# Optimization experiments

Measured on AMD Instinct MI355X. Metric: run time of the kernel, lower is better.

Reference implementation:

```python
import jax, jax.numpy as jnp
import numpy as np

N_NODES = 40000
N_EDGES = 640000
IN_CH = 128
HID_CH = 256
EDGE_DIM = 64
N_SAMP = 2048
T = 1.0
EPS_GIN = 0.0
EPS_NORM = 1e-12


def setup_inputs() -> dict:
    key = jax.random.key(0)
    ks = jax.random.split(key, 12)
    x = jax.random.normal(ks[0], (N_NODES, IN_CH), dtype=jnp.float32)
    edge_index = jax.random.randint(ks[1], (2, N_EDGES), 0, N_NODES, dtype=jnp.int64)
    edge_attr = jax.random.normal(ks[2], (N_EDGES, EDGE_DIM), dtype=jnp.float32)
    pos_ind = jax.random.randint(ks[3], (N_SAMP,), 0, N_NODES, dtype=jnp.int64)
    neg_ind = jax.random.randint(ks[4], (N_SAMP,), 0, N_NODES, dtype=jnp.int64)
    # GINEConv internal edge projection Linear(64 -> 128)
    We = jax.random.normal(ks[5], (EDGE_DIM, IN_CH), dtype=jnp.float32) / np.sqrt(EDGE_DIM)
    be = jnp.zeros((IN_CH,), dtype=jnp.float32)
    # MLP: Linear(128->256), ReLU, Linear(256->256)
    W1 = jax.random.normal(ks[6], (IN_CH, HID_CH), dtype=jnp.float32) / np.sqrt(IN_CH)
    b1 = jnp.zeros((HID_CH,), dtype=jnp.float32)
    W2 = jax.random.normal(ks[7], (HID_CH, HID_CH), dtype=jnp.float32) / np.sqrt(HID_CH)
    b2 = jnp.zeros((HID_CH,), dtype=jnp.float32)
    thresholding_node = jax.random.normal(ks[8], (1, HID_CH), dtype=jnp.float32)
    return {"x": x, "edge_index": edge_index, "edge_attr": edge_attr,
            "pos_ind": pos_ind, "neg_ind": neg_ind,
            "We": We, "be": be, "W1": W1, "b1": b1, "W2": W2, "b2": b2,
            "thresholding_node": thresholding_node}


def _normalize(v):
    n = jnp.linalg.norm(v, axis=-1, keepdims=True)
    return v / jnp.maximum(n, EPS_NORM)


def reference(x, edge_index, edge_attr, pos_ind, neg_ind,
              We, be, W1, b1, W2, b2, thresholding_node):
    src, dst = edge_index[0], edge_index[1]  # PyG: message from x_j (src) to target i (dst)
    edge_emb = edge_attr @ We + be                    # [E, in_ch]
    msg = jax.nn.relu(x[src] + edge_emb)              # gather + add + relu
    agg = jax.ops.segment_sum(msg, dst, num_segments=x.shape[0])  # scatter-add
    h = (1.0 + EPS_GIN) * x + agg
    emb = jax.nn.relu(h @ W1 + b1) @ W2 + b2          # [N, hid]

    center = _normalize(emb[0])                       # [hid]
    pos = _normalize(emb[pos_ind])                    # [P, hid]
    neg = _normalize(emb[neg_ind])                    # [Q, hid]
    thr = _normalize(thresholding_node)               # [1, hid]

    pos_score_mean = (center[None, :] * pos).sum(-1).mean(-1)
    neg_score_mean = (center[None, :] * neg).sum(-1).mean(-1)
    thr_score = (center * thr).sum(-1)                # [1]

    pos_loss = jnp.log(jnp.clip(jax.nn.sigmoid((pos_score_mean - thr_score) / T), 1e-12)).mean()
    neg_loss = jnp.log(jnp.clip(jax.nn.sigmoid((thr_score - neg_score_mean) / T), 1e-12)).mean()
    return -pos_loss - neg_loss
```

## Files before the change

### kernel.cpp

```cpp
#include <hip/hip_runtime.h>
#include <math.h>

#define N_NODES 40000
#define N_EDGES 640000
#define IN_CH 128
#define HID_CH 256
#define EDGE_DIM 64
#define N_SAMP 2048
#define NSEL (1 + 2 * N_SAMP)
#define MAXU 4097
#define HBUCKETS 5120
#define CAP 64
#define MROWS 8

__global__ __launch_bounds__(256) void init_kernel(
    int* __restrict__ slot, int* __restrict__ counters, int* __restrict__ hist)
{
    const int i = blockIdx.x * 256 + threadIdx.x;
    if (i < 40960) slot[i] = -1;
    if (i < HBUCKETS) hist[i] = 0;
    if (i < 32) counters[i] = 0;
}

__global__ __launch_bounds__(256) void flag_kernel(
    const int* __restrict__ pos, const int* __restrict__ neg,
    int* __restrict__ slot, int* __restrict__ counters)
{
    int r = blockIdx.x * 256 + threadIdx.x;
    if (r >= NSEL) return;
    int node = (r == 0) ? 0 : (r <= N_SAMP ? pos[r - 1] : neg[r - 1 - N_SAMP]);
    int old = atomicCAS(&slot[node], -1, -2);
    if (old == -1) slot[node] = atomicAdd(&counters[1], 1);
}

__global__ __launch_bounds__(256) void bucket_kernel(
    const int* __restrict__ ei, const int* __restrict__ slot,
    int* __restrict__ hist, int2* __restrict__ bucket)
{
    const int e = blockIdx.x * 256 + threadIdx.x;
    const int d = ei[N_EDGES + e];
    const int sl = slot[d];
    if (sl >= 0) {
        int p = atomicAdd(&hist[sl], 1);
        if (p < CAP) bucket[(size_t)sl * CAP + p] = make_int2(e, ei[e]);
    }
}

__global__ __launch_bounds__(256) void edge_kernel(
    const float* __restrict__ x, const float* __restrict__ edge_attr,
    const float* __restrict__ We, const float* __restrict__ be,
    const int* __restrict__ hist, const int2* __restrict__ bucket,
    float* __restrict__ agg_c)
{
    __shared__ float sWe[EDGE_DIM * IN_CH];
    __shared__ float sA[4][8][EDGE_DIM];
    __shared__ int scnt[4];
    const int tid = threadIdx.x, wave = tid >> 6, lane = tid & 63;

    {
        const float4* s4 = (const float4*)We;
        float4* d4 = (float4*)sWe;
        for (int i = tid; i < (EDGE_DIM * IN_CH) / 4; i += 256) d4[i] = s4[i];
    }
    const int s = blockIdx.x * 4 + wave;
    const int cnt = min(hist[s], CAP);
    if (lane == 0) scnt[wave] = cnt;
    __syncthreads();
    const int cmax = max(max(scnt[0], scnt[1]), max(scnt[2], scnt[3]));

    const float be0 = be[lane], be1 = be[64 + lane];
    const int2* bk = bucket + (size_t)min(s, MAXU - 1) * CAP;
    float sum0 = 0.f, sum1 = 0.f;

    for (int c0 = 0; c0 < cmax; c0 += 8) {
        int2 bv = make_int2(0, 0);
        {
            int jj = lane & 7;
            if (c0 + jj < cnt) bv = bk[c0 + jj];
        }
#pragma unroll
        for (int j = 0; j < 8; ++j) {
            int e = __shfl(bv.x, j);
            float a = 0.f;
            if (c0 + j < cnt) a = edge_attr[(size_t)e * EDGE_DIM + lane];
            sA[wave][j][lane] = a;
        }
        float xr0[8], xr1[8];
#pragma unroll
        for (int j = 0; j < 8; ++j) {
            int src = __shfl(bv.y, j);
            bool v = (c0 + j < cnt);
            size_t off = (size_t)src * IN_CH;
            xr0[j] = v ? x[off + lane] : 0.f;
            xr1[j] = v ? x[off + 64 + lane] : 0.f;
        }
        __syncthreads();

        float acc0[8], acc1[8];
#pragma unroll
        for (int j = 0; j < 8; ++j) { acc0[j] = 0.f; acc1[j] = 0.f; }
        for (int k0 = 0; k0 < EDGE_DIM; k0 += 4) {
            float w0[4], w1[4];
#pragma unroll
            for (int kk = 0; kk < 4; ++kk) {
                w0[kk] = sWe[(k0 + kk) * IN_CH + lane];
                w1[kk] = sWe[(k0 + kk) * IN_CH + 64 + lane];
            }
#pragma unroll
            for (int j = 0; j < 8; ++j) {
                float4 a = *(const float4*)&sA[wave][j][k0];
                acc0[j] += a.x * w0[0] + a.y * w0[1] + a.z * w0[2] + a.w * w0[3];
                acc1[j] += a.x * w1[0] + a.y * w1[1] + a.z * w1[2] + a.w * w1[3];
            }
        }
#pragma unroll
        for (int j = 0; j < 8; ++j) {
            if (c0 + j < cnt) {
                sum0 += fmaxf(xr0[j] + acc0[j] + be0, 0.f);
                sum1 += fmaxf(xr1[j] + acc1[j] + be1, 0.f);
            }
        }
        __syncthreads();
    }
    agg_c[(size_t)s * IN_CH + lane] = sum0;
    agg_c[(size_t)s * IN_CH + 64 + lane] = sum1;
}

__global__ __launch_bounds__(256) void mlp_kernel(
    const float* __restrict__ x, const float* __restrict__ agg_c,
    const int* __restrict__ slot, const int* __restrict__ pos,
    const int* __restrict__ neg, const float* __restrict__ W1,
    const float* __restrict__ b1, const float* __restrict__ W2,
    const float* __restrict__ b2, float* __restrict__ emb)
{
    __shared__ float sin_[MROWS][IN_CH];
    __shared__ float shid[MROWS][HID_CH];
    __shared__ int snode[MROWS], sslot[MROWS];
    const int tid = threadIdx.x;
    const int r0 = blockIdx.x * MROWS;
    if (tid < MROWS) {
        int r = r0 + tid;
        int node = 0;
        if (r < NSEL && r > 0) node = (r <= N_SAMP) ? pos[r - 1] : neg[r - 1 - N_SAMP];
        snode[tid] = node;
        sslot[tid] = slot[node];
    }
    __syncthreads();
    {
        int rr = tid >> 5, k4 = tid & 31;
        int n = snode[rr], sl = sslot[rr];
        float4 xa = ((const float4*)(x + (size_t)n * IN_CH))[k4];
        float4 ga = ((const float4*)(agg_c + (size_t)sl * IN_CH))[k4];
        ((float4*)sin_[rr])[k4] =
            make_float4(xa.x + ga.x, xa.y + ga.y, xa.z + ga.z, xa.w + ga.w);
    }
    __syncthreads();

    float acc[MROWS];
#pragma unroll
    for (int rr = 0; rr < MROWS; ++rr) acc[rr] = 0.f;
    for (int k0 = 0; k0 < IN_CH; k0 += 4) {
        float w[4];
#pragma unroll
        for (int kk = 0; kk < 4; ++kk) w[kk] = W1[(k0 + kk) * HID_CH + tid];
#pragma unroll
        for (int rr = 0; rr < MROWS; ++rr) {
            float4 h = *(const float4*)&sin_[rr][k0];
            acc[rr] += h.x * w[0] + h.y * w[1] + h.z * w[2] + h.w * w[3];
        }
    }
    float bb1 = b1[tid];
#pragma unroll
    for (int rr = 0; rr < MROWS; ++rr) shid[rr][tid] = fmaxf(acc[rr] + bb1, 0.f);
    __syncthreads();

#pragma unroll
    for (int rr = 0; rr < MROWS; ++rr) acc[rr] = 0.f;
    for (int k0 = 0; k0 < HID_CH; k0 += 4) {
        float w[4];
#pragma unroll
        for (int kk = 0; kk < 4; ++kk) w[kk] = W2[(k0 + kk) * HID_CH + tid];
#pragma unroll
        for (int rr = 0; rr < MROWS; ++rr) {
            float4 h = *(const float4*)&shid[rr][k0];
            acc[rr] += h.x * w[0] + h.y * w[1] + h.z * w[2] + h.w * w[3];
        }
    }
    float bb2 = b2[tid];
#pragma unroll
    for (int rr = 0; rr < MROWS; ++rr) {
        int r = r0 + rr;
        if (r < NSEL) emb[(size_t)r * HID_CH + tid] = acc[rr] + bb2;
    }
}

__global__ __launch_bounds__(256) void score_kernel(
    const float* __restrict__ emb, float* __restrict__ partial)
{
    const int tid = threadIdx.x;
    const int wave = tid >> 6, lane = tid & 63;
    const int rid = blockIdx.x * 4 + wave;
    const float4 c = ((const float4*)emb)[lane];
    const float4 v = ((const float4*)(emb + (size_t)(rid + 1) * HID_CH))[lane];
    float cc = c.x * c.x + c.y * c.y + c.z * c.z + c.w * c.w;
    float vv = v.x * v.x + v.y * v.y + v.z * v.z + v.w * v.w;
    float cv = c.x * v.x + c.y * v.y + c.z * v.z + c.w * v.w;
#pragma unroll
    for (int off = 32; off; off >>= 1) {
        cc += __shfl_xor(cc, off, 64);
        vv += __shfl_xor(vv, off, 64);
        cv += __shfl_xor(cv, off, 64);
    }
    float score = cv / (fmaxf(sqrtf(cc), 1e-12f) * fmaxf(sqrtf(vv), 1e-12f));
    __shared__ float wsum[4];
    if (lane == 0) wsum[wave] = score;
    __syncthreads();
    if (tid == 0) partial[blockIdx.x] = wsum[0] + wsum[1] + wsum[2] + wsum[3];
}

__global__ __launch_bounds__(64) void loss_kernel(
    const float* __restrict__ emb, const float* __restrict__ thrn,
    const float* __restrict__ partial, float* __restrict__ out)
{
    const int lane = threadIdx.x;
    const float4 c = ((const float4*)emb)[lane];
    const float4 t = ((const float4*)thrn)[lane];
    float cc = c.x * c.x + c.y * c.y + c.z * c.z + c.w * c.w;
    float tt = t.x * t.x + t.y * t.y + t.z * t.z + t.w * t.w;
    float ct = c.x * t.x + c.y * t.y + c.z * t.z + c.w * t.w;
    float ps = 0.f, ns = 0.f;
#pragma unroll
    for (int i = 0; i < 8; ++i) ps += partial[lane + 64 * i];
#pragma unroll
    for (int i = 0; i < 8; ++i) ns += partial[512 + lane + 64 * i];
#pragma unroll
    for (int off = 32; off; off >>= 1) {
        cc += __shfl_xor(cc, off, 64);
        tt += __shfl_xor(tt, off, 64);
        ct += __shfl_xor(ct, off, 64);
        ps += __shfl_xor(ps, off, 64);
        ns += __shfl_xor(ns, off, 64);
    }
    if (lane == 0) {
        float thr = ct / (fmaxf(sqrtf(cc), 1e-12f) * fmaxf(sqrtf(tt), 1e-12f));
        float pm = ps / (float)N_SAMP;
        float nm = ns / (float)N_SAMP;
        float s1 = 1.f / (1.f + expf(-(pm - thr)));
        float s2 = 1.f / (1.f + expf(-(thr - nm)));
        s1 = fmaxf(s1, 1e-12f);
        s2 = fmaxf(s2, 1e-12f);
        out[0] = -(logf(s1) + logf(s2));
    }
}

extern "C" void kernel_launch(void* const* d_in, const int* in_sizes, int n_in,
                              void* d_out, int out_size, void* d_ws, size_t ws_size,
                              hipStream_t stream)
{
    const float* x         = (const float*)d_in[0];
    const int*   ei        = (const int*)d_in[1];
    const float* edge_attr = (const float*)d_in[2];
    const int*   pos       = (const int*)d_in[3];
    const int*   neg       = (const int*)d_in[4];
    const float* We        = (const float*)d_in[5];
    const float* be        = (const float*)d_in[6];
    const float* W1        = (const float*)d_in[7];
    const float* b1        = (const float*)d_in[8];
    const float* W2        = (const float*)d_in[9];
    const float* b2        = (const float*)d_in[10];
    const float* thrn      = (const float*)d_in[11];
    float* out = (float*)d_out;

    int* slot     = (int*)d_ws;
    int* counters = slot + 40960;
    int* hist     = counters + 32;
    int2* bucket  = (int2*)(hist + HBUCKETS);
    float* agg_c  = (float*)(bucket + (size_t)MAXU * CAP);
    float* emb    = agg_c + 4100 * IN_CH;
    float* partial= emb + (size_t)NSEL * HID_CH;

    init_kernel<<<160, 256, 0, stream>>>(slot, counters, hist);
    flag_kernel<<<(NSEL + 255) / 256, 256, 0, stream>>>(pos, neg, slot, counters);
    bucket_kernel<<<N_EDGES / 256, 256, 0, stream>>>(ei, slot, hist, bucket);
    edge_kernel<<<1025, 256, 0, stream>>>(x, edge_attr, We, be, hist, bucket, agg_c);
    mlp_kernel<<<(NSEL + MROWS - 1) / MROWS, 256, 0, stream>>>(x, agg_c, slot, pos, neg,
                                                               W1, b1, W2, b2, emb);
    score_kernel<<<1024, 256, 0, stream>>>(emb, partial);
    loss_kernel<<<1, 64, 0, stream>>>(emb, thrn, partial, out);
}
```

Before: 336.7 us.

## Replace block barriers in edge kernel with per-wave sync; fuse loss into score kernel

In the edge aggregation kernel, each wave now loops over its own bucket count and uses its private shared-memory tile. Block-wide __syncthreads inside the loop are replaced by s_waitcnt lgkmcnt(0) plus a scheduling barrier, so waves with few edges no longer wait on the block's maximum. The separate single-block loss kernel is folded into the score kernel, where the last block to finish (found with an atomic counter and threadfence) computes the final loss, saving one launch. The counter-based completion relies on counters being zeroed by init_kernel on every call.

```diff
diff --git a/kernel.cpp b/kernel.cpp
--- a/kernel.cpp
+++ b/kernel.cpp
@@ -54,7 +54,6 @@
 {
     __shared__ float sWe[EDGE_DIM * IN_CH];
     __shared__ float sA[4][8][EDGE_DIM];
-    __shared__ int scnt[4];
     const int tid = threadIdx.x, wave = tid >> 6, lane = tid & 63;
 
     {
@@ -62,17 +61,17 @@
         float4* d4 = (float4*)sWe;
         for (int i = tid; i < (EDGE_DIM * IN_CH) / 4; i += 256) d4[i] = s4[i];
     }
+    __syncthreads();
+
     const int s = blockIdx.x * 4 + wave;
     const int cnt = min(hist[s], CAP);
-    if (lane == 0) scnt[wave] = cnt;
-    __syncthreads();
-    const int cmax = max(max(scnt[0], scnt[1]), max(scnt[2], scnt[3]));
-
     const float be0 = be[lane], be1 = be[64 + lane];
     const int2* bk = bucket + (size_t)min(s, MAXU - 1) * CAP;
+    float (*myA)[EDGE_DIM] = sA[wave];
     float sum0 = 0.f, sum1 = 0.f;
 
-    for (int c0 = 0; c0 < cmax; c0 += 8) {
+    for (int c0 = 0; c0 < cnt; c0 += 8) {
+        asm volatile("s_waitcnt lgkmcnt(0)" ::: "memory");
         int2 bv = make_int2(0, 0);
         {
             int jj = lane & 7;
@@ -83,7 +82,7 @@
             int e = __shfl(bv.x, j);
             float a = 0.f;
             if (c0 + j < cnt) a = edge_attr[(size_t)e * EDGE_DIM + lane];
-            sA[wave][j][lane] = a;
+            myA[j][lane] = a;
         }
         float xr0[8], xr1[8];
 #pragma unroll
@@ -94,7 +93,8 @@
             xr0[j] = v ? x[off + lane] : 0.f;
             xr1[j] = v ? x[off + 64 + lane] : 0.f;
         }
-        __syncthreads();
+        asm volatile("s_waitcnt lgkmcnt(0)" ::: "memory");
+        __builtin_amdgcn_sched_barrier(0);
 
         float acc0[8], acc1[8];
 #pragma unroll
@@ -108,7 +108,7 @@
             }
 #pragma unroll
             for (int j = 0; j < 8; ++j) {
-                float4 a = *(const float4*)&sA[wave][j][k0];
+                float4 a = *(const float4*)&myA[j][k0];
                 acc0[j] += a.x * w0[0] + a.y * w0[1] + a.z * w0[2] + a.w * w0[3];
                 acc1[j] += a.x * w1[0] + a.y * w1[1] + a.z * w1[2] + a.w * w1[3];
             }
@@ -120,7 +120,6 @@
                 sum1 += fmaxf(xr1[j] + acc1[j] + be1, 0.f);
             }
         }
-        __syncthreads();
     }
     agg_c[(size_t)s * IN_CH + lane] = sum0;
     agg_c[(size_t)s * IN_CH + 64 + lane] = sum1;
@@ -195,8 +194,12 @@
 }
 
 __global__ __launch_bounds__(256) void score_kernel(
-    const float* __restrict__ emb, float* __restrict__ partial)
-{
+    const float* __restrict__ emb, const float* __restrict__ thrn,
+    float* __restrict__ partial, int* __restrict__ counters,
+    float* __restrict__ out)
+{
+    __shared__ float wsum[4];
+    __shared__ int sdone;
     const int tid = threadIdx.x;
     const int wave = tid >> 6, lane = tid & 63;
     const int rid = blockIdx.x * 4 + wave;
@@ -212,44 +215,45 @@
         cv += __shfl_xor(cv, off, 64);
     }
     float score = cv / (fmaxf(sqrtf(cc), 1e-12f) * fmaxf(sqrtf(vv), 1e-12f));
-    __shared__ float wsum[4];
     if (lane == 0) wsum[wave] = score;
     __syncthreads();
-    if (tid == 0) partial[blockIdx.x] = wsum[0] + wsum[1] + wsum[2] + wsum[3];
-}
-
-__global__ __launch_bounds__(64) void loss_kernel(
-    const float* __restrict__ emb, const float* __restrict__ thrn,
-    const float* __restrict__ partial, float* __restrict__ out)
-{
-    const int lane = threadIdx.x;
-    const float4 c = ((const float4*)emb)[lane];
-    const float4 t = ((const float4*)thrn)[lane];
-    float cc = c.x * c.x + c.y * c.y + c.z * c.z + c.w * c.w;
-    float tt = t.x * t.x + t.y * t.y + t.z * t.z + t.w * t.w;
-    float ct = c.x * t.x + c.y * t.y + c.z * t.z + c.w * t.w;
-    float ps = 0.f, ns = 0.f;
-#pragma unroll
-    for (int i = 0; i < 8; ++i) ps += partial[lane + 64 * i];
-#pragma unroll
-    for (int i = 0; i < 8; ++i) ns += partial[512 + lane + 64 * i];
-#pragma unroll
-    for (int off = 32; off; off >>= 1) {
-        cc += __shfl_xor(cc, off, 64);
-        tt += __shfl_xor(tt, off, 64);
-        ct += __shfl_xor(ct, off, 64);
-        ps += __shfl_xor(ps, off, 64);
-        ns += __shfl_xor(ns, off, 64);
-    }
-    if (lane == 0) {
-        float thr = ct / (fmaxf(sqrtf(cc), 1e-12f) * fmaxf(sqrtf(tt), 1e-12f));
-        float pm = ps / (float)N_SAMP;
-        float nm = ns / (float)N_SAMP;
-        float s1 = 1.f / (1.f + expf(-(pm - thr)));
-        float s2 = 1.f / (1.f + expf(-(thr - nm)));
-        s1 = fmaxf(s1, 1e-12f);
-        s2 = fmaxf(s2, 1e-12f);
-        out[0] = -(logf(s1) + logf(s2));
+    if (tid == 0) {
+        partial[blockIdx.x] = wsum[0] + wsum[1] + wsum[2] + wsum[3];
+        __threadfence();
+        int old = atomicAdd(&counters[2], 1);
+        sdone = (old == 1023) ? 1 : 0;
+    }
+    __syncthreads();
+    if (sdone && tid < 64) {
+        __threadfence();
+        const float4 cc4 = ((const float4*)emb)[tid];
+        const float4 t = ((const float4*)thrn)[tid];
+        float c2 = cc4.x * cc4.x + cc4.y * cc4.y + cc4.z * cc4.z + cc4.w * cc4.w;
+        float tt = t.x * t.x + t.y * t.y + t.z * t.z + t.w * t.w;
+        float ct = cc4.x * t.x + cc4.y * t.y + cc4.z * t.z + cc4.w * t.w;
+        float ps = 0.f, ns = 0.f;
+#pragma unroll
+        for (int i = 0; i < 8; ++i) ps += partial[tid + 64 * i];
+#pragma unroll
+        for (int i = 0; i < 8; ++i) ns += partial[512 + tid + 64 * i];
+#pragma unroll
+        for (int off = 32; off; off >>= 1) {
+            c2 += __shfl_xor(c2, off, 64);
+            tt += __shfl_xor(tt, off, 64);
+            ct += __shfl_xor(ct, off, 64);
+            ps += __shfl_xor(ps, off, 64);
+            ns += __shfl_xor(ns, off, 64);
+        }
+        if (tid == 0) {
+            float thr = ct / (fmaxf(sqrtf(c2), 1e-12f) * fmaxf(sqrtf(tt), 1e-12f));
+            float pm = ps / (float)N_SAMP;
+            float nm = ns / (float)N_SAMP;
+            float s1 = 1.f / (1.f + expf(-(pm - thr)));
+            float s2 = 1.f / (1.f + expf(-(thr - nm)));
+            s1 = fmaxf(s1, 1e-12f);
+            s2 = fmaxf(s2, 1e-12f);
+            out[0] = -(logf(s1) + logf(s2));
+        }
     }
 }
 
@@ -285,6 +289,5 @@
     edge_kernel<<<1025, 256, 0, stream>>>(x, edge_attr, We, be, hist, bucket, agg_c);
     mlp_kernel<<<(NSEL + MROWS - 1) / MROWS, 256, 0, stream>>>(x, agg_c, slot, pos, neg,
                                                                W1, b1, W2, b2, emb);
-    score_kernel<<<1024, 256, 0, stream>>>(emb, partial);
-    loss_kernel<<<1, 64, 0, stream>>>(emb, thrn, partial, out);
-}
+    score_kernel<<<1024, 256, 0, stream>>>(emb, thrn, partial, counters, out);
+}
```

After: 343.2 us. About the same (+1.9%).
